# Kernel tuning notes

Hardware: AMD Instinct MI355X
Metric: run time of the kernel (lower is better)

Reference implementation:

```python
import jax, jax.numpy as jnp
import numpy as np

B, T, C = 4, 2048, 768
H = 12
D = C // H  # head dim 64

def setup_inputs() -> dict:
    key = jax.random.key(0)
    ks = jax.random.split(key, 6)
    scale = 1.0 / np.sqrt(C)
    x = jax.random.normal(ks[0], (B, T, C), dtype=jnp.float32)
    attention_mask = jax.random.randint(ks[1], (B, T), 0, 2, dtype=jnp.int64)
    Wqkv = jax.random.normal(ks[2], (C, 3 * C), dtype=jnp.float32) * scale
    bqkv = jax.random.normal(ks[3], (3 * C,), dtype=jnp.float32) * 0.02
    Wo = jax.random.normal(ks[4], (C, C), dtype=jnp.float32) * scale
    bo = jax.random.normal(ks[5], (C,), dtype=jnp.float32) * 0.02
    return {"x": x, "attention_mask": attention_mask, "Wqkv": Wqkv,
            "bqkv": bqkv, "Wo": Wo, "bo": bo}

def reference(x, attention_mask, Wqkv, bqkv, Wo, bo):
    # fused QKV projection: [B,T,3C]
    qkv = jnp.einsum('btc,cd->btd', x, Wqkv) + bqkv
    q, k, v = jnp.split(qkv, 3, axis=-1)
    # reshape to [B,H,T,D]
    q = q.reshape(B, T, H, D).transpose(0, 2, 1, 3)
    k = k.reshape(B, T, H, D).transpose(0, 2, 1, 3)
    v = v.reshape(B, T, H, D).transpose(0, 2, 1, 3)
    # module quirk: True (attended) where attention_mask == 0
    keep = (attention_mask == 0)[:, None, None, :]  # [B,1,1,T]
    scores = jnp.einsum('bhqd,bhkd->bhqk', q, k) / np.sqrt(D)
    scores = jnp.where(keep, scores, jnp.finfo(scores.dtype).min)
    probs = jax.nn.softmax(scores, axis=-1)
    context = jnp.einsum('bhqk,bhkd->bhqd', probs, v)
    context = context.transpose(0, 2, 1, 3).reshape(B, T, C)
    return jnp.einsum('btc,cd->btd', context, Wo) + bo
```

## Files before the change

kernel.cpp:

```cpp
#include <hip/hip_runtime.h>
#include <stdint.h>

#define AS1 __attribute__((address_space(1)))
#define AS3 __attribute__((address_space(3)))

typedef _Float16 f16;
typedef _Float16 f16x8 __attribute__((ext_vector_type(8)));
typedef _Float16 f16x4 __attribute__((ext_vector_type(4)));
typedef _Float16 f16x2 __attribute__((ext_vector_type(2)));
typedef float    f32x4  __attribute__((ext_vector_type(4)));
typedef float    f32x16 __attribute__((ext_vector_type(16)));

#define B_  4
#define T_  2048
#define C_  768
#define H_  12
#define D_  64
#define M_  (B_*T_)
#define N1_ (3*C_)

__device__ __forceinline__ void g2l16(const void* g, void* l) {
  __builtin_amdgcn_global_load_lds((const AS1 void*)g, (AS3 void*)l, 16, 0, 0);
}

__device__ __forceinline__ f32x4 fzero4() { f32x4 z = {0.f, 0.f, 0.f, 0.f}; return z; }

__device__ __forceinline__ f16x2 pk_f16(float a, float b) {
  auto t = __builtin_amdgcn_cvt_pkrtz(a, b);
  return *(f16x2*)&t;
}

__global__ __launch_bounds__(256)
void transpose_cvt_k(const float* __restrict__ in, f16* __restrict__ out, int R, int C) {
  __shared__ float tile[32][33];
  const int tx = threadIdx.x & 31, ty = threadIdx.x >> 5;
  const int c0 = blockIdx.x * 32, r0 = blockIdx.y * 32;
#pragma unroll
  for (int i = 0; i < 32; i += 8)
    tile[ty + i][tx] = in[(long)(r0 + ty + i) * C + c0 + tx];
  __syncthreads();
#pragma unroll
  for (int i = 0; i < 32; i += 8)
    out[(long)(c0 + ty + i) * R + r0 + tx] = (f16)tile[tx][ty + i];
}

__global__ __launch_bounds__(256)
void convert_f32_f16(const float* __restrict__ in, f16* __restrict__ out) {
  const int i = (blockIdx.x * 256 + threadIdx.x) * 4;
  const float4 v = *(const float4*)(in + i);
  f16x4 o = {(f16)v.x, (f16)v.y, (f16)v.z, (f16)v.w};
  *(f16x4*)(out + i) = o;
}

__global__ __launch_bounds__(256)
void init_idx_kernel(int* __restrict__ idx, int* __restrict__ cnt) {
  const int g = blockIdx.x * 256 + threadIdx.x;
  idx[g] = 0;
  if (g < B_) cnt[g] = 0;
}

__global__ __launch_bounds__(256)
void compact_kernel(const int* __restrict__ mask, int* __restrict__ idx,
                    int* __restrict__ cnt) {
  const int b = blockIdx.y;
  const int t = blockIdx.x * 256 + threadIdx.x;
  if (mask[b * T_ + t] == 0) {
    const int s = atomicAdd(&cnt[b], 1);
    idx[b * T_ + s] = t;
  }
}

__global__ __launch_bounds__(256)
void build_vt_gather(const f16* __restrict__ qkv, const int* __restrict__ idx,
                     const int* __restrict__ cnt, f16* __restrict__ vt) {
  __shared__ f16 tile[32][33];
  const int z = blockIdx.z, b = z / H_, h = z % H_;
  const int s0 = blockIdx.x * 32, d0 = blockIdx.y * 32;
  if (s0 >= cnt[b]) return;
  const int tx = threadIdx.x & 31, ty = threadIdx.x >> 5;
  const int* idx_b = idx + b * T_;
  f16* dst = vt + (long)z * D_ * T_;
#pragma unroll
  for (int i = 0; i < 32; i += 8) {
    const int t = idx_b[s0 + ty + i];
    tile[ty + i][tx] = qkv[(long)(b * T_ + t) * N1_ + 2 * C_ + h * D_ + d0 + tx];
  }
  __syncthreads();
#pragma unroll
  for (int i = 0; i < 32; i += 8)
    dst[(long)(d0 + ty + i) * T_ + s0 + tx] = tile[tx][ty + i];
}

template <typename OutT>
__global__ __launch_bounds__(256)
void gemm_bias_kernel(const f16* __restrict__ A, const f16* __restrict__ Bt,
                      const float* __restrict__ bias, OutT* __restrict__ Cc,
                      int K, int ldc) {
  __shared__ f16 lA[128 * 32];
  __shared__ f16 lB[128 * 32];
  const int tid = threadIdx.x;
  const int n0 = blockIdx.x * 128, m0 = blockIdx.y * 128;
  const int lane = tid & 63, w = tid >> 6;
  const int wm = (w & 1) * 64, wn = (w >> 1) * 64;
  const int r15 = lane & 15, q4 = lane >> 4;

  const int c0 = tid, c1 = 256 + tid;
  const int ar0 = c0 >> 2, ak0 = (c0 & 3) * 8;
  const int ar1 = c1 >> 2, ak1 = (c1 & 3) * 8;
  const f16* Ab = A + (long)m0 * K;
  const f16* Bb = Bt + (long)n0 * K;

  f32x4 acc[4][4];
#pragma unroll
  for (int i = 0; i < 4; i++)
#pragma unroll
    for (int j = 0; j < 4; j++) acc[i][j] = fzero4();

  for (int kb = 0; kb < K; kb += 32) {
    g2l16(Ab + (long)ar0 * K + kb + ak0, &lA[c0 * 8]);
    g2l16(Ab + (long)ar1 * K + kb + ak1, &lA[c1 * 8]);
    g2l16(Bb + (long)ar0 * K + kb + ak0, &lB[c0 * 8]);
    g2l16(Bb + (long)ar1 * K + kb + ak1, &lB[c1 * 8]);
    __syncthreads();
    f16x8 af[4], bfv[4];
#pragma unroll
    for (int mi = 0; mi < 4; mi++)
      af[mi] = *(const f16x8*)&lA[(wm + mi * 16 + r15) * 32 + q4 * 8];
#pragma unroll
    for (int ni = 0; ni < 4; ni++)
      bfv[ni] = *(const f16x8*)&lB[(wn + ni * 16 + r15) * 32 + q4 * 8];
#pragma unroll
    for (int mi = 0; mi < 4; mi++)
#pragma unroll
      for (int ni = 0; ni < 4; ni++)
        acc[mi][ni] = __builtin_amdgcn_mfma_f32_16x16x32_f16(af[mi], bfv[ni], acc[mi][ni], 0, 0, 0);
    __syncthreads();
  }

#pragma unroll
  for (int ni = 0; ni < 4; ni++) {
    const int col = n0 + wn + ni * 16 + r15;
    const float bs = bias[col];
#pragma unroll
    for (int mi = 0; mi < 4; mi++) {
#pragma unroll
      for (int r = 0; r < 4; r++) {
        const int row = m0 + wm + mi * 16 + q4 * 4 + r;
        Cc[(long)row * ldc + col] = (OutT)(acc[mi][ni][r] + bs);
      }
    }
  }
}

__global__ __launch_bounds__(256, 4)
void attn_kernel(const f16* __restrict__ qkv, const f16* __restrict__ vtc,
                 const int* __restrict__ idx, const int* __restrict__ cnt,
                 f16* __restrict__ ctx) {
  const int LDS_ = 72;
  __shared__ f16 QPs[128 * 72];
  __shared__ f16 Ks[64 * 72], Vs[64 * 72];
  const int tid = threadIdx.x, lane = tid & 63, w = tid >> 6;
  const int l31 = lane & 31, hh = lane >> 5;
  const int bh = blockIdx.y, b = bh / H_, h = bh % H_;
  const int q0 = blockIdx.x * 128;
  const f16* Qg = qkv + (long)(b * T_ + q0) * N1_ + h * D_;
  const f16* Kbase = qkv + (long)b * T_ * N1_ + C_ + h * D_;
  const f16* Vg = vtc + (long)bh * D_ * T_;
  const int* idx_b = idx + b * T_;
  const int nk = cnt[b];
  const int nkt = (nk + 63) >> 6;

  const f16 qsc = (f16)0.18033688f;
#pragma unroll
  for (int i = 0; i < 4; i++) {
    int c = i * 256 + tid, r = c >> 3, dcq = (c & 7) * 8;
    f16x8 v = *(const f16x8*)(Qg + (long)r * N1_ + dcq);
#pragma unroll
    for (int j = 0; j < 8; j++) v[j] = v[j] * qsc;
    *(f16x8*)&QPs[r * LDS_ + dcq] = v;
  }
  __syncthreads();
  f16x8 bq[4];
#pragma unroll
  for (int j = 0; j < 4; j++)
    bq[j] = *(const f16x8*)&QPs[(w * 32 + l31) * LDS_ + j * 16 + hh * 8];

  const int r0 = tid >> 3, r1 = 32 + (tid >> 3), dc = (tid & 7) * 8;
  int idxp0 = idx_b[r0], idxp1 = idx_b[r1];

  float l_acc = 0.f;
  f32x16 O[2];
#pragma unroll
  for (int dt = 0; dt < 2; dt++)
#pragma unroll
    for (int r = 0; r < 16; r++) O[dt][r] = 0.f;

  for (int kt = 0; kt < (nkt << 6); kt += 64) {
    __syncthreads();
    {
      const int t0 = idxp0, t1 = idxp1;
      f16x8 kv0 = *(const f16x8*)(Kbase + (long)t0 * N1_ + dc);
      f16x8 kv1 = *(const f16x8*)(Kbase + (long)t1 * N1_ + dc);
      f16x8 vv0 = *(const f16x8*)(Vg + (long)r0 * T_ + kt + dc);
      f16x8 vv1 = *(const f16x8*)(Vg + (long)r1 * T_ + kt + dc);
      idxp0 = idx_b[min(kt + 64 + r0, T_ - 1)];
      idxp1 = idx_b[min(kt + 64 + r1, T_ - 1)];
      *(f16x8*)&Ks[r0 * LDS_ + dc] = kv0;
      *(f16x8*)&Ks[r1 * LDS_ + dc] = kv1;
      *(f16x8*)&Vs[r0 * LDS_ + dc] = vv0;
      *(f16x8*)&Vs[r1 * LDS_ + dc] = vv1;
    }
    __syncthreads();

    const bool full = (kt + 64 <= nk);
#pragma unroll
    for (int ktile = 0; ktile < 2; ktile++) {
      f32x16 acc;
      if (full) {
#pragma unroll
        for (int r = 0; r < 16; r++) acc[r] = 0.f;
      } else {
        const int kbase = kt + ktile * 32 + hh * 4;
#pragma unroll
        for (int g = 0; g < 4; g++)
#pragma unroll
          for (int i = 0; i < 4; i++)
            acc[4 * g + i] = (kbase + 8 * g + i < nk) ? 0.f : -1e30f;
      }
#pragma unroll
      for (int j = 0; j < 4; j++) {
        f16x8 ak = *(const f16x8*)&Ks[(ktile * 32 + l31) * LDS_ + j * 16 + hh * 8];
        acc = __builtin_amdgcn_mfma_f32_32x32x16_f16(ak, bq[j], acc, 0, 0, 0);
      }
#pragma unroll
      for (int g = 0; g < 4; g++) {
        const float p0 = __builtin_amdgcn_exp2f(acc[4 * g + 0]);
        const float p1 = __builtin_amdgcn_exp2f(acc[4 * g + 1]);
        const float p2 = __builtin_amdgcn_exp2f(acc[4 * g + 2]);
        const float p3 = __builtin_amdgcn_exp2f(acc[4 * g + 3]);
        l_acc += (p0 + p1) + (p2 + p3);
        const f16x2 lo = pk_f16(p0, p1), hi = pk_f16(p2, p3);
        f16x4 pv; pv[0] = lo[0]; pv[1] = lo[1]; pv[2] = hi[0]; pv[3] = hi[1];
        *(f16x4*)&QPs[(w * 32 + l31) * LDS_ + ktile * 32 + g * 8 + hh * 4] = pv;
      }
    }
    asm volatile("s_waitcnt lgkmcnt(0)" ::: "memory");

#pragma unroll
    for (int j = 0; j < 4; j++) {
      f16x8 pa = *(const f16x8*)&QPs[(w * 32 + l31) * LDS_ + j * 16 + hh * 8];
#pragma unroll
      for (int dt = 0; dt < 2; dt++) {
        f16x8 vb = *(const f16x8*)&Vs[(dt * 32 + l31) * LDS_ + j * 16 + hh * 8];
        O[dt] = __builtin_amdgcn_mfma_f32_32x32x16_f16(pa, vb, O[dt], 0, 0, 0);
      }
    }
  }

  l_acc += __shfl_xor(l_acc, 32);
  float* Lw = (float*)&QPs[(w * 32) * LDS_];
  asm volatile("s_waitcnt lgkmcnt(0)" ::: "memory");
  if (hh == 0) Lw[l31] = l_acc;
  asm volatile("s_waitcnt lgkmcnt(0)" ::: "memory");
#pragma unroll
  for (int g = 0; g < 4; g++) {
    const f32x4 lv = *(const f32x4*)&Lw[g * 8 + hh * 4];
#pragma unroll
    for (int i = 0; i < 4; i++) {
      const float inv = 1.f / lv[i];
      const int row = b * T_ + q0 + w * 32 + g * 8 + hh * 4 + i;
#pragma unroll
      for (int dt = 0; dt < 2; dt++)
        ctx[(long)row * C_ + h * D_ + dt * 32 + l31] = (f16)(O[dt][4 * g + i] * inv);
    }
  }
}

extern "C" void kernel_launch(void* const* d_in, const int* in_sizes, int n_in,
                              void* d_out, int out_size, void* d_ws, size_t ws_size,
                              hipStream_t stream) {
  (void)in_sizes; (void)n_in; (void)out_size; (void)ws_size;
  const float* x    = (const float*)d_in[0];
  const int*   mask = (const int*)  d_in[1];
  const float* Wqkv = (const float*)d_in[2];
  const float* bqkv = (const float*)d_in[3];
  const float* Wo   = (const float*)d_in[4];
  const float* bo   = (const float*)d_in[5];
  float* out = (float*)d_out;

  char* ws = (char*)d_ws;
  const size_t OFF_WQKVT = 0;
  const size_t OFF_WOT   = OFF_WQKVT + 3538944;
  const size_t OFF_QKV   = OFF_WOT + 1179648;
  const size_t OFF_VT    = OFF_QKV + 37748736;
  const size_t OFF_XH    = OFF_VT + 12582912;
  const size_t OFF_IDX   = OFF_XH + 12582912;
  const size_t OFF_CNT   = OFF_IDX + 32768;
  f16* WqkvT = (f16*)(ws + OFF_WQKVT);
  f16* WoT   = (f16*)(ws + OFF_WOT);
  f16* qkv   = (f16*)(ws + OFF_QKV);
  f16* Vtc   = (f16*)(ws + OFF_VT);
  f16* xh    = (f16*)(ws + OFF_XH);
  f16* ctx   = (f16*)(ws + OFF_XH);
  int* idx   = (int*)(ws + OFF_IDX);
  int* cnt   = (int*)(ws + OFF_CNT);

  transpose_cvt_k<<<dim3(72, 24), 256, 0, stream>>>(Wqkv, WqkvT, 768, 2304);
  transpose_cvt_k<<<dim3(24, 24), 256, 0, stream>>>(Wo, WoT, 768, 768);
  convert_f32_f16<<<dim3(M_ * C_ / 1024), 256, 0, stream>>>(x, xh);
  init_idx_kernel<<<dim3(B_ * T_ / 256), 256, 0, stream>>>(idx, cnt);
  compact_kernel<<<dim3(T_ / 256, B_), 256, 0, stream>>>(mask, idx, cnt);
  gemm_bias_kernel<f16><<<dim3(18, 64), 256, 0, stream>>>(xh, WqkvT, bqkv, qkv, 768, 2304);
  build_vt_gather<<<dim3(64, 2, 48), 256, 0, stream>>>(qkv, idx, cnt, Vtc);
  attn_kernel<<<dim3(16, 48), 256, 0, stream>>>(qkv, Vtc, idx, cnt, ctx);
  gemm_bias_kernel<float><<<dim3(6, 64), 256, 0, stream>>>(ctx, WoT, bo, out, 768, 768);
}
```

Baseline: 219.2 us.

## Fuse x conversion into QKV GEMM, restructure attention with split-K waves and pre-swizzled V

The f32-to-f16 conversion of x moves into the QKV GEMM's A-tile load, and index init merges into a single-block-per-batch compaction kernel, which removes two launches and an intermediate buffer. The attention kernel now uses 32-query blocks of two waves. Each wave processes alternate key tiles, reading K straight from global memory and V from a layout pre-swizzled into MFMA fragment order by build_vt_gather. The two waves' partial outputs and row sums are then combined through LDS. This drops the shared K/V staging and its barriers, at the cost of uncoalesced gathered K loads from global memory and an extra reduction step.

```diff
diff --git a/kernel.cpp b/kernel.cpp
--- a/kernel.cpp
+++ b/kernel.cpp
@@ -45,55 +45,58 @@
 }
 
 __global__ __launch_bounds__(256)
-void convert_f32_f16(const float* __restrict__ in, f16* __restrict__ out) {
-  const int i = (blockIdx.x * 256 + threadIdx.x) * 4;
-  const float4 v = *(const float4*)(in + i);
-  f16x4 o = {(f16)v.x, (f16)v.y, (f16)v.z, (f16)v.w};
-  *(f16x4*)(out + i) = o;
-}
-
-__global__ __launch_bounds__(256)
-void init_idx_kernel(int* __restrict__ idx, int* __restrict__ cnt) {
-  const int g = blockIdx.x * 256 + threadIdx.x;
-  idx[g] = 0;
-  if (g < B_) cnt[g] = 0;
-}
-
-__global__ __launch_bounds__(256)
 void compact_kernel(const int* __restrict__ mask, int* __restrict__ idx,
                     int* __restrict__ cnt) {
-  const int b = blockIdx.y;
-  const int t = blockIdx.x * 256 + threadIdx.x;
-  if (mask[b * T_ + t] == 0) {
-    const int s = atomicAdd(&cnt[b], 1);
-    idx[b * T_ + s] = t;
-  }
+  __shared__ int c_l;
+  const int b = blockIdx.x;
+  if (threadIdx.x == 0) c_l = 0;
+  __syncthreads();
+#pragma unroll
+  for (int i = 0; i < T_ / 256; i++) {
+    const int t = i * 256 + threadIdx.x;
+    if (mask[b * T_ + t] == 0) {
+      const int s = atomicAdd(&c_l, 1);
+      idx[b * T_ + s] = t;
+    }
+  }
+  __syncthreads();
+  const int nk = c_l;
+  for (int s = nk + threadIdx.x; s < T_; s += 256) idx[b * T_ + s] = 0;
+  if (threadIdx.x == 0) cnt[b] = nk;
 }
 
 __global__ __launch_bounds__(256)
 void build_vt_gather(const f16* __restrict__ qkv, const int* __restrict__ idx,
                      const int* __restrict__ cnt, f16* __restrict__ vt) {
-  __shared__ f16 tile[32][33];
+  __shared__ f16 tile2[32][40];
   const int z = blockIdx.z, b = z / H_, h = z % H_;
   const int s0 = blockIdx.x * 32, d0 = blockIdx.y * 32;
   if (s0 >= cnt[b]) return;
   const int tx = threadIdx.x & 31, ty = threadIdx.x >> 5;
   const int* idx_b = idx + b * T_;
-  f16* dst = vt + (long)z * D_ * T_;
 #pragma unroll
   for (int i = 0; i < 32; i += 8) {
     const int t = idx_b[s0 + ty + i];
-    tile[ty + i][tx] = qkv[(long)(b * T_ + t) * N1_ + 2 * C_ + h * D_ + d0 + tx];
-  }
-  __syncthreads();
-#pragma unroll
-  for (int i = 0; i < 32; i += 8)
-    dst[(long)(d0 + ty + i) * T_ + s0 + tx] = tile[tx][ty + i];
-}
-
-template <typename OutT>
+    tile2[tx][ty + i] = qkv[(long)(b * T_ + t) * N1_ + 2 * C_ + h * D_ + d0 + tx];
+  }
+  __syncthreads();
+  if (threadIdx.x < 128) {
+    const int l31 = threadIdx.x & 31;
+    const int hh  = (threadIdx.x >> 5) & 1;
+    const int jj  = (threadIdx.x >> 6) & 1;
+    const int dt = d0 >> 5;
+    const int j  = ((s0 & 32) >> 4) + jj;
+    const int kloc = jj * 16 + hh * 8;
+    f16x8 v = *(const f16x8*)&tile2[l31][kloc];
+    f16* dst = vt + (long)z * D_ * T_ + (long)(s0 >> 6) * 4096
+             + ((dt * 4 + j) * 64 + hh * 32 + l31) * 8;
+    *(f16x8*)dst = v;
+  }
+}
+
+template <typename OutT, bool CVT>
 __global__ __launch_bounds__(256)
-void gemm_bias_kernel(const f16* __restrict__ A, const f16* __restrict__ Bt,
+void gemm_bias_kernel(const void* __restrict__ Ap, const f16* __restrict__ Bt,
                       const float* __restrict__ bias, OutT* __restrict__ Cc,
                       int K, int ldc) {
   __shared__ f16 lA[128 * 32];
@@ -107,7 +110,8 @@
   const int c0 = tid, c1 = 256 + tid;
   const int ar0 = c0 >> 2, ak0 = (c0 & 3) * 8;
   const int ar1 = c1 >> 2, ak1 = (c1 & 3) * 8;
-  const f16* Ab = A + (long)m0 * K;
+  const f16*   Ab = CVT ? nullptr : (const f16*)Ap + (long)m0 * K;
+  const float* Af = CVT ? (const float*)Ap + (long)m0 * K : nullptr;
   const f16* Bb = Bt + (long)n0 * K;
 
   f32x4 acc[4][4];
@@ -117,8 +121,22 @@
     for (int j = 0; j < 4; j++) acc[i][j] = fzero4();
 
   for (int kb = 0; kb < K; kb += 32) {
-    g2l16(Ab + (long)ar0 * K + kb + ak0, &lA[c0 * 8]);
-    g2l16(Ab + (long)ar1 * K + kb + ak1, &lA[c1 * 8]);
+    if constexpr (CVT) {
+      const float* p0 = Af + (long)ar0 * K + kb + ak0;
+      const float* p1 = Af + (long)ar1 * K + kb + ak1;
+      float4 u0 = *(const float4*)p0, u1 = *(const float4*)(p0 + 4);
+      float4 u2 = *(const float4*)p1, u3 = *(const float4*)(p1 + 4);
+      f16x8 v0, v1;
+      v0[0]=(f16)u0.x; v0[1]=(f16)u0.y; v0[2]=(f16)u0.z; v0[3]=(f16)u0.w;
+      v0[4]=(f16)u1.x; v0[5]=(f16)u1.y; v0[6]=(f16)u1.z; v0[7]=(f16)u1.w;
+      v1[0]=(f16)u2.x; v1[1]=(f16)u2.y; v1[2]=(f16)u2.z; v1[3]=(f16)u2.w;
+      v1[4]=(f16)u3.x; v1[5]=(f16)u3.y; v1[6]=(f16)u3.z; v1[7]=(f16)u3.w;
+      *(f16x8*)&lA[c0 * 8] = v0;
+      *(f16x8*)&lA[c1 * 8] = v1;
+    } else {
+      g2l16(Ab + (long)ar0 * K + kb + ak0, &lA[c0 * 8]);
+      g2l16(Ab + (long)ar1 * K + kb + ak1, &lA[c1 * 8]);
+    }
     g2l16(Bb + (long)ar0 * K + kb + ak0, &lB[c0 * 8]);
     g2l16(Bb + (long)ar1 * K + kb + ak1, &lB[c1 * 8]);
     __syncthreads();
@@ -152,41 +170,33 @@
   }
 }
 
-__global__ __launch_bounds__(256, 4)
+__global__ __launch_bounds__(128, 5)
 void attn_kernel(const f16* __restrict__ qkv, const f16* __restrict__ vtc,
                  const int* __restrict__ idx, const int* __restrict__ cnt,
                  f16* __restrict__ ctx) {
-  const int LDS_ = 72;
-  __shared__ f16 QPs[128 * 72];
-  __shared__ f16 Ks[64 * 72], Vs[64 * 72];
+  const int P_LDS = 72;
+  __shared__ f16 Ps[2 * 32 * 72];
   const int tid = threadIdx.x, lane = tid & 63, w = tid >> 6;
   const int l31 = lane & 31, hh = lane >> 5;
   const int bh = blockIdx.y, b = bh / H_, h = bh % H_;
-  const int q0 = blockIdx.x * 128;
+  const int q0 = blockIdx.x * 32;
   const f16* Qg = qkv + (long)(b * T_ + q0) * N1_ + h * D_;
   const f16* Kbase = qkv + (long)b * T_ * N1_ + C_ + h * D_;
   const f16* Vg = vtc + (long)bh * D_ * T_;
   const int* idx_b = idx + b * T_;
   const int nk = cnt[b];
   const int nkt = (nk + 63) >> 6;
+  f16* Pw = Ps + w * 32 * P_LDS;
 
   const f16 qsc = (f16)0.18033688f;
-#pragma unroll
-  for (int i = 0; i < 4; i++) {
-    int c = i * 256 + tid, r = c >> 3, dcq = (c & 7) * 8;
-    f16x8 v = *(const f16x8*)(Qg + (long)r * N1_ + dcq);
-#pragma unroll
-    for (int j = 0; j < 8; j++) v[j] = v[j] * qsc;
-    *(f16x8*)&QPs[r * LDS_ + dcq] = v;
-  }
-  __syncthreads();
   f16x8 bq[4];
 #pragma unroll
-  for (int j = 0; j < 4; j++)
-    bq[j] = *(const f16x8*)&QPs[(w * 32 + l31) * LDS_ + j * 16 + hh * 8];
-
-  const int r0 = tid >> 3, r1 = 32 + (tid >> 3), dc = (tid & 7) * 8;
-  int idxp0 = idx_b[r0], idxp1 = idx_b[r1];
+  for (int j = 0; j < 4; j++) {
+    f16x8 v = *(const f16x8*)(Qg + (long)l31 * N1_ + j * 16 + hh * 8);
+#pragma unroll
+    for (int e = 0; e < 8; e++) v[e] *= qsc;
+    bq[j] = v;
+  }
 
   float l_acc = 0.f;
   f32x16 O[2];
@@ -195,26 +205,14 @@
 #pragma unroll
     for (int r = 0; r < 16; r++) O[dt][r] = 0.f;
 
-  for (int kt = 0; kt < (nkt << 6); kt += 64) {
-    __syncthreads();
-    {
-      const int t0 = idxp0, t1 = idxp1;
-      f16x8 kv0 = *(const f16x8*)(Kbase + (long)t0 * N1_ + dc);
-      f16x8 kv1 = *(const f16x8*)(Kbase + (long)t1 * N1_ + dc);
-      f16x8 vv0 = *(const f16x8*)(Vg + (long)r0 * T_ + kt + dc);
-      f16x8 vv1 = *(const f16x8*)(Vg + (long)r1 * T_ + kt + dc);
-      idxp0 = idx_b[min(kt + 64 + r0, T_ - 1)];
-      idxp1 = idx_b[min(kt + 64 + r1, T_ - 1)];
-      *(f16x8*)&Ks[r0 * LDS_ + dc] = kv0;
-      *(f16x8*)&Ks[r1 * LDS_ + dc] = kv1;
-      *(f16x8*)&Vs[r0 * LDS_ + dc] = vv0;
-      *(f16x8*)&Vs[r1 * LDS_ + dc] = vv1;
-    }
-    __syncthreads();
-
+  for (int it = w; it < nkt; it += 2) {
+    const int kt = it * 64;
     const bool full = (kt + 64 <= nk);
+    const int t0 = idx_b[kt + l31];
+    const int t1 = idx_b[kt + 32 + l31];
 #pragma unroll
     for (int ktile = 0; ktile < 2; ktile++) {
+      const long tk = (ktile ? t1 : t0);
       f32x16 acc;
       if (full) {
 #pragma unroll
@@ -229,7 +227,7 @@
       }
 #pragma unroll
       for (int j = 0; j < 4; j++) {
-        f16x8 ak = *(const f16x8*)&Ks[(ktile * 32 + l31) * LDS_ + j * 16 + hh * 8];
+        f16x8 ak = *(const f16x8*)(Kbase + tk * N1_ + j * 16 + hh * 8);
         acc = __builtin_amdgcn_mfma_f32_32x32x16_f16(ak, bq[j], acc, 0, 0, 0);
       }
 #pragma unroll
@@ -241,37 +239,52 @@
         l_acc += (p0 + p1) + (p2 + p3);
         const f16x2 lo = pk_f16(p0, p1), hi = pk_f16(p2, p3);
         f16x4 pv; pv[0] = lo[0]; pv[1] = lo[1]; pv[2] = hi[0]; pv[3] = hi[1];
-        *(f16x4*)&QPs[(w * 32 + l31) * LDS_ + ktile * 32 + g * 8 + hh * 4] = pv;
+        *(f16x4*)&Pw[l31 * P_LDS + ktile * 32 + g * 8 + hh * 4] = pv;
       }
     }
     asm volatile("s_waitcnt lgkmcnt(0)" ::: "memory");
 
+    const f16* Vtile = Vg + (long)(kt >> 6) * 4096;
 #pragma unroll
     for (int j = 0; j < 4; j++) {
-      f16x8 pa = *(const f16x8*)&QPs[(w * 32 + l31) * LDS_ + j * 16 + hh * 8];
+      f16x8 pa = *(const f16x8*)&Pw[l31 * P_LDS + j * 16 + hh * 8];
 #pragma unroll
       for (int dt = 0; dt < 2; dt++) {
-        f16x8 vb = *(const f16x8*)&Vs[(dt * 32 + l31) * LDS_ + j * 16 + hh * 8];
+        f16x8 vb = *(const f16x8*)(Vtile + ((dt * 4 + j) * 64 + lane) * 8);
         O[dt] = __builtin_amdgcn_mfma_f32_32x32x16_f16(pa, vb, O[dt], 0, 0, 0);
       }
     }
   }
 
   l_acc += __shfl_xor(l_acc, 32);
-  float* Lw = (float*)&QPs[(w * 32) * LDS_];
+  const int ow = 1 - w;
+  f32x16 Okeep, Ogive;
+#pragma unroll
+  for (int r = 0; r < 16; r++) {
+    Okeep[r] = (w == 0) ? O[0][r] : O[1][r];
+    Ogive[r] = (w == 0) ? O[1][r] : O[0][r];
+  }
+  float* Ex = (float*)Ps;
+  float* Lb = Ex + 2048;
+  float* Lfin = Lb + 64;
+  __syncthreads();
+#pragma unroll
+  for (int r = 0; r < 16; r++) Ex[ow * 1024 + lane * 16 + r] = Ogive[r];
+  if (hh == 0) Lb[w * 32 + l31] = l_acc;
+  __syncthreads();
+#pragma unroll
+  for (int r = 0; r < 16; r++) Okeep[r] += Ex[w * 1024 + lane * 16 + r];
+  const float ltot = l_acc + Lb[ow * 32 + l31];
+  if (hh == 0) Lfin[w * 32 + l31] = ltot;
   asm volatile("s_waitcnt lgkmcnt(0)" ::: "memory");
-  if (hh == 0) Lw[l31] = l_acc;
-  asm volatile("s_waitcnt lgkmcnt(0)" ::: "memory");
 #pragma unroll
   for (int g = 0; g < 4; g++) {
-    const f32x4 lv = *(const f32x4*)&Lw[g * 8 + hh * 4];
+    const f32x4 lv = *(const f32x4*)&Lfin[w * 32 + g * 8 + hh * 4];
 #pragma unroll
     for (int i = 0; i < 4; i++) {
       const float inv = 1.f / lv[i];
-      const int row = b * T_ + q0 + w * 32 + g * 8 + hh * 4 + i;
-#pragma unroll
-      for (int dt = 0; dt < 2; dt++)
-        ctx[(long)row * C_ + h * D_ + dt * 32 + l31] = (f16)(O[dt][4 * g + i] * inv);
+      const int row = b * T_ + q0 + g * 8 + hh * 4 + i;
+      ctx[(long)row * C_ + h * D_ + w * 32 + l31] = (f16)(Okeep[4 * g + i] * inv);
     }
   }
 }
@@ -293,25 +306,22 @@
   const size_t OFF_WOT   = OFF_WQKVT + 3538944;
   const size_t OFF_QKV   = OFF_WOT + 1179648;
   const size_t OFF_VT    = OFF_QKV + 37748736;
-  const size_t OFF_XH    = OFF_VT + 12582912;
-  const size_t OFF_IDX   = OFF_XH + 12582912;
+  const size_t OFF_CTX   = OFF_VT + 12582912;
+  const size_t OFF_IDX   = OFF_CTX + 12582912;
   const size_t OFF_CNT   = OFF_IDX + 32768;
   f16* WqkvT = (f16*)(ws + OFF_WQKVT);
   f16* WoT   = (f16*)(ws + OFF_WOT);
   f16* qkv   = (f16*)(ws + OFF_QKV);
   f16* Vtc   = (f16*)(ws + OFF_VT);
-  f16* xh    = (f16*)(ws + OFF_XH);
-  f16* ctx   = (f16*)(ws + OFF_XH);
+  f16* ctx   = (f16*)(ws + OFF_CTX);
   int* idx   = (int*)(ws + OFF_IDX);
   int* cnt   = (int*)(ws + OFF_CNT);
 
   transpose_cvt_k<<<dim3(72, 24), 256, 0, stream>>>(Wqkv, WqkvT, 768, 2304);
   transpose_cvt_k<<<dim3(24, 24), 256, 0, stream>>>(Wo, WoT, 768, 768);
-  convert_f32_f16<<<dim3(M_ * C_ / 1024), 256, 0, stream>>>(x, xh);
-  init_idx_kernel<<<dim3(B_ * T_ / 256), 256, 0, stream>>>(idx, cnt);
-  compact_kernel<<<dim3(T_ / 256, B_), 256, 0, stream>>>(mask, idx, cnt);
-  gemm_bias_kernel<f16><<<dim3(18, 64), 256, 0, stream>>>(xh, WqkvT, bqkv, qkv, 768, 2304);
+  compact_kernel<<<dim3(B_), 256, 0, stream>>>(mask, idx, cnt);
+  gemm_bias_kernel<f16, true><<<dim3(18, 64), 256, 0, stream>>>(x, WqkvT, bqkv, qkv, 768, 2304);
   build_vt_gather<<<dim3(64, 2, 48), 256, 0, stream>>>(qkv, idx, cnt, Vtc);
-  attn_kernel<<<dim3(16, 48), 256, 0, stream>>>(qkv, Vtc, idx, cnt, ctx);
-  gemm_bias_kernel<float><<<dim3(6, 64), 256, 0, stream>>>(ctx, WoT, bo, out, 768, 768);
-}
+  attn_kernel<<<dim3(64, 48), 128, 0, stream>>>(qkv, Vtc, idx, cnt, ctx);
+  gemm_bias_kernel<float, false><<<dim3(6, 64), 256, 0, stream>>>(ctx, WoT, bo, out, 768, 768);
+}
```

Result: slower. 279.6 us (+27.6%).
